# Performance work log

Measured on AMD Instinct MI355X. Metric: run time of the kernel, lower is better.

## Reference

```python
import jax, jax.numpy as jnp
import numpy as np

B, S, HID = 2, 2048, 2048
H, KVH, HD = 16, 8, 128
EPS = 1e-6
ROPE_THETA = 1e6
NEG = -1e9


def setup_inputs() -> dict:
    key = jax.random.key(0)
    ks = jax.random.split(key, 8)
    hidden_states = jax.random.normal(ks[0], (B, S, HID), dtype=jnp.float32)
    # real rotary embeddings, HF layout: concat(freqs, freqs) along last dim
    inv_freq = 1.0 / (ROPE_THETA ** (jnp.arange(0, HD, 2, dtype=jnp.float32) / HD))
    freqs = jnp.arange(S, dtype=jnp.float32)[:, None] * inv_freq[None, :]  # [S, HD/2]
    emb = jnp.concatenate([freqs, freqs], axis=-1)  # [S, HD]
    cos = jnp.broadcast_to(jnp.cos(emb)[None], (B, S, HD)).astype(jnp.float32)
    sin = jnp.broadcast_to(jnp.sin(emb)[None], (B, S, HD)).astype(jnp.float32)
    # additive causal mask [B, 1, S, S]
    causal = jnp.tril(jnp.ones((S, S), dtype=bool))
    attention_mask = jnp.broadcast_to(
        jnp.where(causal, 0.0, NEG).astype(jnp.float32)[None, None], (B, 1, S, S)
    )
    sc_in = 1.0 / np.sqrt(HID)
    sc_o = 1.0 / np.sqrt(H * HD)
    q_kernel = jax.random.normal(ks[1], (HID, H * HD), dtype=jnp.float32) * sc_in
    k_kernel = jax.random.normal(ks[2], (HID, KVH * HD), dtype=jnp.float32) * sc_in
    v_kernel = jax.random.normal(ks[3], (HID, KVH * HD), dtype=jnp.float32) * sc_in
    o_kernel = jax.random.normal(ks[4], (H * HD, HID), dtype=jnp.float32) * sc_o
    q_norm_w = jnp.ones((HD,), dtype=jnp.float32)
    k_norm_w = jnp.ones((HD,), dtype=jnp.float32)
    return dict(hidden_states=hidden_states, cos=cos, sin=sin,
                attention_mask=attention_mask, q_kernel=q_kernel, k_kernel=k_kernel,
                v_kernel=v_kernel, o_kernel=o_kernel, q_norm_w=q_norm_w, k_norm_w=k_norm_w)


def _rms_norm(x, w):
    dt = x.dtype
    xf = x.astype(jnp.float32)
    var = jnp.mean(jnp.square(xf), axis=-1, keepdims=True)
    return (w * (xf * jax.lax.rsqrt(var + EPS))).astype(dt)


def _rotate_half(x):
    x1, x2 = jnp.split(x, 2, axis=-1)
    return jnp.concatenate([-x2, x1], axis=-1)


def _apply_rope(q, k, cos, sin):
    # q,k: [B,H,S,HD]; cos,sin: [B,S,HD] -> unsqueeze head dim
    cos = cos[:, None, :, :]
    sin = sin[:, None, :, :]
    q = q * cos + _rotate_half(q) * sin
    k = k * cos + _rotate_half(k) * sin
    return q, k


def reference(hidden_states, cos, sin, attention_mask, q_kernel, k_kernel,
              v_kernel, o_kernel, q_norm_w, k_norm_w):
    b, s, _ = hidden_states.shape
    groups = H // KVH
    scaling = HD ** -0.5

    q = (hidden_states @ q_kernel).reshape(b, s, H, HD).transpose(0, 2, 1, 3)
    k = (hidden_states @ k_kernel).reshape(b, s, KVH, HD).transpose(0, 2, 1, 3)
    v = (hidden_states @ v_kernel).reshape(b, s, KVH, HD).transpose(0, 2, 1, 3)

    q = _rms_norm(q, q_norm_w)
    k = _rms_norm(k, k_norm_w)
    q, k = _apply_rope(q, k, cos, sin)

    # GQA repeat_kv: [B,KVH,S,HD] -> [B,H,S,HD]
    k = jnp.repeat(k, groups, axis=1)
    v = jnp.repeat(v, groups, axis=1)

    attn = jnp.einsum('bhqd,bhkd->bhqk', q, k) * scaling  # [B,H,S,S]
    attn = attn + jnp.broadcast_to(attention_mask[:, :, :, :s], (b, H, s, s))
    attn = jax.nn.softmax(attn, axis=-1)
    out = jnp.einsum('bhqk,bhkd->bhqd', attn, v)
    out = out.transpose(0, 2, 1, 3).reshape(b, s, H * HD)
    return out @ o_kernel
```

## Files before the change

kernel.cpp:

```cpp
#include <hip/hip_runtime.h>
#include <hip/hip_bf16.h>
#include <stdint.h>

#define S_ 2048
#define H_ 16
#define KVH_ 8
#define HD_ 128

typedef short bf16x8 __attribute__((ext_vector_type(8)));
typedef float f32x4 __attribute__((ext_vector_type(4)));

__device__ __forceinline__ unsigned short f2bf(float f) {
    union { float f; uint32_t u; } v; v.f = f;
    uint32_t u = v.u;
    return (unsigned short)((u + 0x7FFFu + ((u >> 16) & 1u)) >> 16);
}
__device__ __forceinline__ float bf2f(unsigned short s) {
    union { uint32_t u; float f; } v; v.u = ((uint32_t)s) << 16;
    return v.f;
}
__device__ __forceinline__ void gload16(const void* g, void* l) {
    __builtin_amdgcn_global_load_lds(
        (const __attribute__((address_space(1))) unsigned int*)(uintptr_t)g,
        (__attribute__((address_space(3))) unsigned int*)(unsigned int)(uintptr_t)l,
        16, 0, 0);
}
__device__ __forceinline__ float rowred_sum(float x) {
    float t;
    t = __int_as_float(__builtin_amdgcn_update_dpp(0, __float_as_int(x), 0x121, 0xF, 0xF, true)); x += t;
    t = __int_as_float(__builtin_amdgcn_update_dpp(0, __float_as_int(x), 0x122, 0xF, 0xF, true)); x += t;
    t = __int_as_float(__builtin_amdgcn_update_dpp(0, __float_as_int(x), 0x124, 0xF, 0xF, true)); x += t;
    t = __int_as_float(__builtin_amdgcn_update_dpp(0, __float_as_int(x), 0x128, 0xF, 0xF, true)); x += t;
    return x;
}

__global__ __launch_bounds__(256) void k_prep(
    const float* __restrict__ hidden, unsigned short* __restrict__ Xb,
    const float* __restrict__ qk, const float* __restrict__ kk,
    const float* __restrict__ vk, const float* __restrict__ ok,
    unsigned short* __restrict__ Wqkvt, unsigned short* __restrict__ Wot) {
    const int tid = threadIdx.x;
    if (blockIdx.x < 2048) {
        int i = blockIdx.x * 256 + tid;
        const int stride = 2048 * 256;
        #pragma unroll
        for (int u = 0; u < 4; u++, i += stride) {
            float4 f = ((const float4*)hidden)[i];
            ushort4 o;
            o.x = f2bf(f.x); o.y = f2bf(f.y); o.z = f2bf(f.z); o.w = f2bf(f.w);
            ((ushort4*)Xb)[i] = o;
        }
    } else {
        __shared__ float tile[32][33];
        const int t = blockIdx.x - 2048;
        const float* src; unsigned short* dst; int N, bx, by;
        if (t < 4096)      { src = qk; dst = Wqkvt;                          N = 2048; bx = t & 63; by = t >> 6; }
        else if (t < 6144) { int u = t - 4096; src = kk; dst = Wqkvt + (size_t)2048 * 2048; N = 1024; bx = u & 31; by = u >> 5; }
        else if (t < 8192) { int u = t - 6144; src = vk; dst = Wqkvt + (size_t)3072 * 2048; N = 1024; bx = u & 31; by = u >> 5; }
        else               { int u = t - 8192; src = ok; dst = Wot;          N = 2048; bx = u & 63; by = u >> 6; }
        const int n0 = bx * 32, k0 = by * 32;
        const int tx = tid & 31, ty = tid >> 5;
        #pragma unroll
        for (int j = 0; j < 32; j += 8)
            tile[ty + j][tx] = src[(size_t)(k0 + ty + j) * N + n0 + tx];
        __syncthreads();
        #pragma unroll
        for (int j = 0; j < 32; j += 8)
            dst[(size_t)(n0 + ty + j) * 2048 + k0 + tx] = f2bf(tile[tx][ty + j]);
    }
}

template <int BM, int OUT_F32>
__global__ __launch_bounds__(512) void k_gemm256(const unsigned short* __restrict__ A,
                                                 const unsigned short* __restrict__ Bt,
                                                 void* __restrict__ Cv,
                                                 int M, int N, int K) {
    __shared__ __align__(16) unsigned short As[2][BM * 32];
    __shared__ __align__(16) unsigned short Bs[2][256 * 32];
    const int tid = threadIdx.x;
    const int wave = tid >> 6, lane = tid & 63;
    const int lm = lane & 15, lg = lane >> 4;
    const int wr = wave >> 2, wc = wave & 3;
    const int m0 = blockIdx.y * BM, n0 = blockIdx.x * 256;
    constexpr int MF = BM / 32;
    f32x4 acc[MF][4] = {};
    const int srow = wave * 16 + (lane >> 2);
    const int sslot = (lane & 3) ^ ((lane >> 3) & 3);
    const unsigned short* gA = A + (size_t)(m0 + srow) * K + sslot * 8;
    const unsigned short* gB = Bt + (size_t)(n0 + srow) * K + sslot * 8;
    const int swz = lg ^ ((lm >> 1) & 3);
    const int NKT = K >> 5;

    auto STAGE = [&](int kt, int buf) {
        const int c = kt * 32;
        char* lA = (char*)&As[buf][0] + wave * 1024;
        char* lB = (char*)&Bs[buf][0] + wave * 1024;
        gload16(gA + c, lA);
        if constexpr (BM == 256) gload16(gA + c + (size_t)128 * K, lA + 8192);
        gload16(gB + c, lB);
        gload16(gB + c + (size_t)128 * K, lB + 8192);
    };
    STAGE(0, 0);
    for (int kt = 0; kt < NKT; ++kt) {
        const int cur = kt & 1;
        if (kt + 1 < NKT) {
            STAGE(kt + 1, cur ^ 1);
            __builtin_amdgcn_sched_barrier(0);
            if constexpr (BM == 256) asm volatile("s_waitcnt vmcnt(4)" ::: "memory");
            else                     asm volatile("s_waitcnt vmcnt(3)" ::: "memory");
        } else {
            __builtin_amdgcn_sched_barrier(0);
            asm volatile("s_waitcnt vmcnt(0)" ::: "memory");
        }
        __builtin_amdgcn_s_barrier();
        __builtin_amdgcn_sched_barrier(0);
        bf16x8 bfr[4];
        #pragma unroll
        for (int n = 0; n < 4; n++)
            bfr[n] = *(const bf16x8*)&Bs[cur][(wc * 64 + n * 16 + lm) * 32 + swz * 8];
        __builtin_amdgcn_s_setprio(1);
        #pragma unroll
        for (int m = 0; m < MF; m++) {
            bf16x8 a = *(const bf16x8*)&As[cur][(wr * (BM / 2) + m * 16 + lm) * 32 + swz * 8];
            #pragma unroll
            for (int n = 0; n < 4; n++)
                acc[m][n] = __builtin_amdgcn_mfma_f32_16x16x32_bf16(a, bfr[n], acc[m][n], 0, 0, 0);
        }
        __builtin_amdgcn_s_setprio(0);
        __builtin_amdgcn_sched_barrier(0);
        __builtin_amdgcn_s_barrier();
        __builtin_amdgcn_sched_barrier(0);
    }
    #pragma unroll
    for (int m = 0; m < MF; m++) {
        const int row = m0 + wr * (BM / 2) + m * 16 + lg * 4;
        #pragma unroll
        for (int n = 0; n < 4; n++) {
            const int col = n0 + wc * 64 + n * 16 + lm;
            #pragma unroll
            for (int i = 0; i < 4; i++) {
                if (OUT_F32) ((float*)Cv)[(size_t)(row + i) * N + col] = acc[m][n][i];
                else ((unsigned short*)Cv)[(size_t)(row + i) * N + col] = f2bf(acc[m][n][i]);
            }
        }
    }
}

__global__ __launch_bounds__(256) void k_normvt(
    const unsigned short* __restrict__ Cqkv,
    const float* __restrict__ cosb, const float* __restrict__ sinb,
    const float* __restrict__ qw, const float* __restrict__ kw,
    unsigned short* __restrict__ Qb, unsigned short* __restrict__ Kb,
    unsigned short* __restrict__ Vtg) {
    const int tid = threadIdx.x;
    if (blockIdx.x < 4096) {
        const int row = blockIdx.x;
        const int b = row >> 11, s = row & (S_ - 1);
        const int wave = tid >> 6, lane = tid & 63;
        const float c0 = cosb[(size_t)row * HD_ + lane];
        const float c1 = cosb[(size_t)row * HD_ + lane + 64];
        const float s0 = sinb[(size_t)row * HD_ + lane];
        const float s1 = sinb[(size_t)row * HD_ + lane + 64];
        for (int u = wave; u < 24; u += 4) {
            const int isq = (u < 16);
            const int head = isq ? u : u - 16;
            const unsigned short* x = Cqkv + (size_t)row * 4096 + (isq ? 0 : 2048) + head * HD_;
            float x0 = bf2f(x[lane]), x1 = bf2f(x[lane + 64]);
            float ss = x0 * x0 + x1 * x1;
            #pragma unroll
            for (int o = 32; o >= 1; o >>= 1) ss += __shfl_xor(ss, o, 64);
            float r = rsqrtf(ss * (1.0f / HD_) + 1e-6f);
            const float* wv = isq ? qw : kw;
            float y0 = x0 * r * wv[lane], y1 = x1 * r * wv[lane + 64];
            float o0 = y0 * c0 - y1 * s0;
            float o1 = y1 * c1 + y0 * s1;
            unsigned short* dst = isq ? Qb + ((size_t)(b * H_ + head) * S_ + s) * HD_
                                      : Kb + ((size_t)(b * KVH_ + head) * S_ + s) * HD_;
            dst[lane] = f2bf(o0);
            dst[lane + 64] = f2bf(o1);
        }
    } else {
        __shared__ unsigned short tile[32][34];
        const int t = blockIdx.x - 4096;
        const int x = t & 63, y = (t >> 6) & 3, bkh = t >> 8;
        const int b = bkh >> 3, kh = bkh & 7;
        const int s0 = x * 32, d0 = y * 32;
        const int tx = tid & 31, ty = tid >> 5;
        #pragma unroll
        for (int j = 0; j < 32; j += 8)
            tile[ty + j][tx] = Cqkv[(size_t)(b * S_ + s0 + ty + j) * 4096 + 3072 + kh * HD_ + d0 + tx];
        __syncthreads();
        #pragma unroll
        for (int j = 0; j < 32; j += 8)
            Vtg[((size_t)bkh * HD_ + d0 + ty + j) * S_ + s0 + tx] = tile[tx][ty + j];
    }
}

__global__ __launch_bounds__(256) void k_attn(
    const unsigned short* __restrict__ Qb,
    const unsigned short* __restrict__ Kb,
    const unsigned short* __restrict__ Vtg,
    unsigned short* __restrict__ AO) {
    __shared__ __align__(16) unsigned short Kt[2][64 * 128];
    __shared__ __align__(16) unsigned short Vt[2][128 * 64];
    __shared__ __align__(16) unsigned short Pl[4][16][72];
    const int h = blockIdx.y, b = blockIdx.z;
    const int qi = (b == 0) ? (gridDim.x - 1 - blockIdx.x) : blockIdx.x;
    const int kh = h >> 1;
    const int tid = threadIdx.x, wave = tid >> 6, lane = tid & 63;
    const int lm = lane & 15, lg = lane >> 4;
    const int q0 = qi * 128;
    bf16x8 qf[2][4];
    #pragma unroll
    for (int rg = 0; rg < 2; rg++) {
        const unsigned short* Qp = Qb + ((size_t)(b * H_ + h) * S_ + q0 + wave * 32 + rg * 16 + lm) * HD_;
        #pragma unroll
        for (int d0 = 0; d0 < 4; d0++) qf[rg][d0] = *(const bf16x8*)(Qp + d0 * 32 + lg * 8);
    }
    f32x4 accO[2][8] = {};
    float lrow[2][4];
    #pragma unroll
    for (int rg = 0; rg < 2; rg++)
        #pragma unroll
        for (int i = 0; i < 4; i++) lrow[rg][i] = 0.f;
    const unsigned short* Kg = Kb + (size_t)(b * KVH_ + kh) * S_ * HD_;
    const unsigned short* Vg = Vtg + (size_t)(b * KVH_ + kh) * HD_ * S_;
    const int kr = wave * 4 + (lane >> 4);
    const int kc = ((lane & 15) ^ (kr & 7)) * 8;
    const int vr = wave * 8 + (lane >> 3);
    const int vc = ((lane & 7) ^ (vr & 7)) * 8;
    const float scaling = 0.08838834764831845f;
    const int NT = 2 * qi + 2;

    auto STAGE = [&](int t, int buf) {
        const int k0 = t * 64;
        char* lK = (char*)&Kt[buf][0] + wave * 1024;
        char* lV = (char*)&Vt[buf][0] + wave * 1024;
        #pragma unroll
        for (int j = 0; j < 4; ++j) {
            gload16(Kg + (size_t)(k0 + kr + j * 16) * HD_ + kc, lK + j * 4096);
            gload16(Vg + (size_t)(vr + j * 32) * S_ + k0 + vc, lV + j * 4096);
        }
    };
    STAGE(0, 0);
    for (int t = 0; t < NT; ++t) {
        const int cur = t & 1;
        const int k0 = t * 64;
        if (t + 1 < NT) {
            STAGE(t + 1, cur ^ 1);
            __builtin_amdgcn_sched_barrier(0);
            asm volatile("s_waitcnt vmcnt(8)" ::: "memory");
        } else {
            __builtin_amdgcn_sched_barrier(0);
            asm volatile("s_waitcnt vmcnt(0)" ::: "memory");
        }
        __builtin_amdgcn_s_barrier();
        __builtin_amdgcn_sched_barrier(0);
        f32x4 sc[2][4] = {};
        __builtin_amdgcn_s_setprio(1);
        #pragma unroll
        for (int nk = 0; nk < 4; nk++)
            #pragma unroll
            for (int d0 = 0; d0 < 4; d0++) {
                bf16x8 kf = *(const bf16x8*)&Kt[cur][(nk * 16 + lm) * 128 +
                                                    ((d0 * 32 + lg * 8) ^ ((lm & 7) << 3))];
                sc[0][nk] = __builtin_amdgcn_mfma_f32_16x16x32_bf16(qf[0][d0], kf, sc[0][nk], 0, 0, 0);
                sc[1][nk] = __builtin_amdgcn_mfma_f32_16x16x32_bf16(qf[1][d0], kf, sc[1][nk], 0, 0, 0);
            }
        __builtin_amdgcn_s_setprio(0);
        const bool diag = (t >= 2 * qi);
        #pragma unroll
        for (int rg = 0; rg < 2; rg++) {
            const int qrow0 = q0 + wave * 32 + rg * 16;
            float rs[4] = { 0.f, 0.f, 0.f, 0.f };
            #pragma unroll
            for (int nk = 0; nk < 4; nk++)
                #pragma unroll
                for (int i = 0; i < 4; i++) {
                    float v = sc[rg][nk][i] * scaling;
                    if (diag && (k0 + nk * 16 + lm) > (qrow0 + lg * 4 + i)) v = -1e30f;
                    float p = __expf(v);
                    rs[i] += p;
                    Pl[wave][lg * 4 + i][nk * 16 + lm] = f2bf(p);
                }
            #pragma unroll
            for (int i = 0; i < 4; i++) rs[i] = rowred_sum(rs[i]);
            #pragma unroll
            for (int i = 0; i < 4; i++) lrow[rg][i] += rs[i];
            __builtin_amdgcn_s_setprio(1);
            #pragma unroll
            for (int kk = 0; kk < 2; kk++) {
                bf16x8 pa = *(const bf16x8*)&Pl[wave][lm][kk * 32 + lg * 8];
                #pragma unroll
                for (int df = 0; df < 8; df++) {
                    bf16x8 vf = *(const bf16x8*)&Vt[cur][(df * 16 + lm) * 64 +
                                                         ((kk * 32 + lg * 8) ^ ((lm & 7) << 3))];
                    accO[rg][df] = __builtin_amdgcn_mfma_f32_16x16x32_bf16(pa, vf, accO[rg][df], 0, 0, 0);
                }
            }
            __builtin_amdgcn_s_setprio(0);
        }
        __builtin_amdgcn_sched_barrier(0);
        __builtin_amdgcn_s_barrier();
        __builtin_amdgcn_sched_barrier(0);
    }
    #pragma unroll
    for (int rg = 0; rg < 2; rg++) {
        unsigned short* Op = AO + ((size_t)b * S_ + q0 + wave * 32 + rg * 16) * (H_ * HD_) + h * HD_;
        #pragma unroll
        for (int df = 0; df < 8; df++)
            #pragma unroll
            for (int i = 0; i < 4; i++) {
                float v = accO[rg][df][i] / lrow[rg][i];
                Op[(size_t)(lg * 4 + i) * (H_ * HD_) + df * 16 + lm] = f2bf(v);
            }
    }
}

extern "C" void kernel_launch(void* const* d_in, const int* in_sizes, int n_in,
                              void* d_out, int out_size, void* d_ws, size_t ws_size,
                              hipStream_t stream) {
    const float* hidden = (const float*)d_in[0];
    const float* cosb = (const float*)d_in[1];
    const float* sinb = (const float*)d_in[2];
    const float* qk = (const float*)d_in[4];
    const float* kk = (const float*)d_in[5];
    const float* vk = (const float*)d_in[6];
    const float* ok = (const float*)d_in[7];
    const float* qw = (const float*)d_in[8];
    const float* kw = (const float*)d_in[9];
    char* ws = (char*)d_ws;
    unsigned short* Xb    = (unsigned short*)ws;
    unsigned short* Wqkvt = (unsigned short*)(ws + (16u << 20));
    unsigned short* Wot   = (unsigned short*)(ws + (32u << 20));
    unsigned short* Cqkv  = (unsigned short*)(ws + (40u << 20));
    unsigned short* Qb  = Xb;
    unsigned short* Kb  = Wqkvt;
    unsigned short* Vtg = (unsigned short*)(ws + (24u << 20));
    unsigned short* AO  = Cqkv;

    k_prep<<<14336, 256, 0, stream>>>(hidden, Xb, qk, kk, vk, ok, Wqkvt, Wot);
    k_gemm256<256, 0><<<dim3(16, 16), 512, 0, stream>>>(Xb, Wqkvt, Cqkv, 4096, 4096, 2048);
    k_normvt<<<8192, 256, 0, stream>>>(Cqkv, cosb, sinb, qw, kw, Qb, Kb, Vtg);
    k_attn<<<dim3(16, H_, 2), 256, 0, stream>>>(Qb, Kb, Vtg, AO);
    k_gemm256<128, 1><<<dim3(8, 32), 512, 0, stream>>>(AO, Wot, d_out, 4096, 2048, 2048);
}
```

Before: 239.5 us.

## Halve attention query tile and split K/V staging into single-buffered interleaved loads

```diff
diff --git a/kernel.cpp b/kernel.cpp
--- a/kernel.cpp
+++ b/kernel.cpp
@@ -201,28 +201,21 @@
     const unsigned short* __restrict__ Kb,
     const unsigned short* __restrict__ Vtg,
     unsigned short* __restrict__ AO) {
-    __shared__ __align__(16) unsigned short Kt[2][64 * 128];
-    __shared__ __align__(16) unsigned short Vt[2][128 * 64];
+    __shared__ __align__(16) unsigned short Kt[64 * 128];
+    __shared__ __align__(16) unsigned short Vt[128 * 64];
     __shared__ __align__(16) unsigned short Pl[4][16][72];
     const int h = blockIdx.y, b = blockIdx.z;
-    const int qi = (b == 0) ? (gridDim.x - 1 - blockIdx.x) : blockIdx.x;
+    const int qi = gridDim.x - 1 - blockIdx.x;
     const int kh = h >> 1;
     const int tid = threadIdx.x, wave = tid >> 6, lane = tid & 63;
     const int lm = lane & 15, lg = lane >> 4;
-    const int q0 = qi * 128;
-    bf16x8 qf[2][4];
+    const int q0 = qi * 64;
+    const unsigned short* Qp = Qb + ((size_t)(b * H_ + h) * S_ + q0 + wave * 16 + lm) * HD_;
+    bf16x8 qf[4];
     #pragma unroll
-    for (int rg = 0; rg < 2; rg++) {
-        const unsigned short* Qp = Qb + ((size_t)(b * H_ + h) * S_ + q0 + wave * 32 + rg * 16 + lm) * HD_;
-        #pragma unroll
-        for (int d0 = 0; d0 < 4; d0++) qf[rg][d0] = *(const bf16x8*)(Qp + d0 * 32 + lg * 8);
-    }
-    f32x4 accO[2][8] = {};
-    float lrow[2][4];
-    #pragma unroll
-    for (int rg = 0; rg < 2; rg++)
-        #pragma unroll
-        for (int i = 0; i < 4; i++) lrow[rg][i] = 0.f;
+    for (int d0 = 0; d0 < 4; d0++) qf[d0] = *(const bf16x8*)(Qp + d0 * 32 + lg * 8);
+    f32x4 accO[8] = {};
+    float lrow[4] = { 0.f, 0.f, 0.f, 0.f };
     const unsigned short* Kg = Kb + (size_t)(b * KVH_ + kh) * S_ * HD_;
     const unsigned short* Vg = Vtg + (size_t)(b * KVH_ + kh) * HD_ * S_;
     const int kr = wave * 4 + (lane >> 4);
@@ -230,91 +223,92 @@
     const int vr = wave * 8 + (lane >> 3);
     const int vc = ((lane & 7) ^ (vr & 7)) * 8;
     const float scaling = 0.08838834764831845f;
-    const int NT = 2 * qi + 2;
-
-    auto STAGE = [&](int t, int buf) {
+    const int NT = qi + 1;
+
+    auto STAGE_K = [&](int t) {
         const int k0 = t * 64;
-        char* lK = (char*)&Kt[buf][0] + wave * 1024;
-        char* lV = (char*)&Vt[buf][0] + wave * 1024;
-        #pragma unroll
-        for (int j = 0; j < 4; ++j) {
+        char* lK = (char*)&Kt[0] + wave * 1024;
+        #pragma unroll
+        for (int j = 0; j < 4; ++j)
             gload16(Kg + (size_t)(k0 + kr + j * 16) * HD_ + kc, lK + j * 4096);
+    };
+    auto STAGE_V = [&](int t) {
+        const int k0 = t * 64;
+        char* lV = (char*)&Vt[0] + wave * 1024;
+        #pragma unroll
+        for (int j = 0; j < 4; ++j)
             gload16(Vg + (size_t)(vr + j * 32) * S_ + k0 + vc, lV + j * 4096);
-        }
     };
-    STAGE(0, 0);
+    STAGE_K(0);
+    STAGE_V(0);
     for (int t = 0; t < NT; ++t) {
-        const int cur = t & 1;
         const int k0 = t * 64;
-        if (t + 1 < NT) {
-            STAGE(t + 1, cur ^ 1);
-            __builtin_amdgcn_sched_barrier(0);
-            asm volatile("s_waitcnt vmcnt(8)" ::: "memory");
-        } else {
-            __builtin_amdgcn_sched_barrier(0);
-            asm volatile("s_waitcnt vmcnt(0)" ::: "memory");
-        }
-        __builtin_amdgcn_s_barrier();
-        __builtin_amdgcn_sched_barrier(0);
-        f32x4 sc[2][4] = {};
+        __builtin_amdgcn_sched_barrier(0);
+        asm volatile("s_waitcnt vmcnt(4)" ::: "memory");
+        __builtin_amdgcn_s_barrier();
+        __builtin_amdgcn_sched_barrier(0);
+        f32x4 sc[4] = {};
         __builtin_amdgcn_s_setprio(1);
         #pragma unroll
         for (int nk = 0; nk < 4; nk++)
             #pragma unroll
             for (int d0 = 0; d0 < 4; d0++) {
-                bf16x8 kf = *(const bf16x8*)&Kt[cur][(nk * 16 + lm) * 128 +
-                                                    ((d0 * 32 + lg * 8) ^ ((lm & 7) << 3))];
-                sc[0][nk] = __builtin_amdgcn_mfma_f32_16x16x32_bf16(qf[0][d0], kf, sc[0][nk], 0, 0, 0);
-                sc[1][nk] = __builtin_amdgcn_mfma_f32_16x16x32_bf16(qf[1][d0], kf, sc[1][nk], 0, 0, 0);
+                bf16x8 kf = *(const bf16x8*)&Kt[(nk * 16 + lm) * 128 +
+                                               ((d0 * 32 + lg * 8) ^ ((lm & 7) << 3))];
+                sc[nk] = __builtin_amdgcn_mfma_f32_16x16x32_bf16(qf[d0], kf, sc[nk], 0, 0, 0);
             }
         __builtin_amdgcn_s_setprio(0);
-        const bool diag = (t >= 2 * qi);
-        #pragma unroll
-        for (int rg = 0; rg < 2; rg++) {
-            const int qrow0 = q0 + wave * 32 + rg * 16;
-            float rs[4] = { 0.f, 0.f, 0.f, 0.f };
-            #pragma unroll
-            for (int nk = 0; nk < 4; nk++)
-                #pragma unroll
-                for (int i = 0; i < 4; i++) {
-                    float v = sc[rg][nk][i] * scaling;
-                    if (diag && (k0 + nk * 16 + lm) > (qrow0 + lg * 4 + i)) v = -1e30f;
-                    float p = __expf(v);
-                    rs[i] += p;
-                    Pl[wave][lg * 4 + i][nk * 16 + lm] = f2bf(p);
-                }
-            #pragma unroll
-            for (int i = 0; i < 4; i++) rs[i] = rowred_sum(rs[i]);
-            #pragma unroll
-            for (int i = 0; i < 4; i++) lrow[rg][i] += rs[i];
-            __builtin_amdgcn_s_setprio(1);
-            #pragma unroll
-            for (int kk = 0; kk < 2; kk++) {
-                bf16x8 pa = *(const bf16x8*)&Pl[wave][lm][kk * 32 + lg * 8];
-                #pragma unroll
-                for (int df = 0; df < 8; df++) {
-                    bf16x8 vf = *(const bf16x8*)&Vt[cur][(df * 16 + lm) * 64 +
-                                                         ((kk * 32 + lg * 8) ^ ((lm & 7) << 3))];
-                    accO[rg][df] = __builtin_amdgcn_mfma_f32_16x16x32_bf16(pa, vf, accO[rg][df], 0, 0, 0);
-                }
+        __builtin_amdgcn_sched_barrier(0);
+        __builtin_amdgcn_s_barrier();
+        __builtin_amdgcn_sched_barrier(0);
+        if (t + 1 < NT) STAGE_K(t + 1);
+        const bool diag = (t == qi);
+        const int qrow0 = q0 + wave * 16;
+        float rs[4] = { 0.f, 0.f, 0.f, 0.f };
+        #pragma unroll
+        for (int nk = 0; nk < 4; nk++)
+            #pragma unroll
+            for (int i = 0; i < 4; i++) {
+                float v = sc[nk][i] * scaling;
+                if (diag && (k0 + nk * 16 + lm) > (qrow0 + lg * 4 + i)) v = -1e30f;
+                float p = __expf(v);
+                rs[i] += p;
+                Pl[wave][lg * 4 + i][nk * 16 + lm] = f2bf(p);
             }
-            __builtin_amdgcn_s_setprio(0);
-        }
-        __builtin_amdgcn_sched_barrier(0);
-        __builtin_amdgcn_s_barrier();
-        __builtin_amdgcn_sched_barrier(0);
-    }
+        #pragma unroll
+        for (int i = 0; i < 4; i++) rs[i] = rowred_sum(rs[i]);
+        #pragma unroll
+        for (int i = 0; i < 4; i++) lrow[i] += rs[i];
+        __builtin_amdgcn_sched_barrier(0);
+        if (t + 1 < NT) { asm volatile("s_waitcnt vmcnt(4)" ::: "memory"); }
+        else            { asm volatile("s_waitcnt vmcnt(0)" ::: "memory"); }
+        __builtin_amdgcn_s_barrier();
+        __builtin_amdgcn_sched_barrier(0);
+        __builtin_amdgcn_s_setprio(1);
+        #pragma unroll
+        for (int kk = 0; kk < 2; kk++) {
+            bf16x8 pa = *(const bf16x8*)&Pl[wave][lm][kk * 32 + lg * 8];
+            #pragma unroll
+            for (int df = 0; df < 8; df++) {
+                bf16x8 vf = *(const bf16x8*)&Vt[(df * 16 + lm) * 64 +
+                                               ((kk * 32 + lg * 8) ^ ((lm & 7) << 3))];
+                accO[df] = __builtin_amdgcn_mfma_f32_16x16x32_bf16(pa, vf, accO[df], 0, 0, 0);
+            }
+        }
+        __builtin_amdgcn_s_setprio(0);
+        __builtin_amdgcn_sched_barrier(0);
+        __builtin_amdgcn_s_barrier();
+        __builtin_amdgcn_sched_barrier(0);
+        if (t + 1 < NT) STAGE_V(t + 1);
+    }
+    unsigned short* Op = AO + ((size_t)b * S_ + q0 + wave * 16) * (H_ * HD_) + h * HD_;
     #pragma unroll
-    for (int rg = 0; rg < 2; rg++) {
-        unsigned short* Op = AO + ((size_t)b * S_ + q0 + wave * 32 + rg * 16) * (H_ * HD_) + h * HD_;
-        #pragma unroll
-        for (int df = 0; df < 8; df++)
-            #pragma unroll
-            for (int i = 0; i < 4; i++) {
-                float v = accO[rg][df][i] / lrow[rg][i];
-                Op[(size_t)(lg * 4 + i) * (H_ * HD_) + df * 16 + lm] = f2bf(v);
-            }
-    }
+    for (int df = 0; df < 8; df++)
+        #pragma unroll
+        for (int i = 0; i < 4; i++) {
+            float v = accO[df][i] / lrow[i];
+            Op[(size_t)(lg * 4 + i) * (H_ * HD_) + df * 16 + lm] = f2bf(v);
+        }
 }
 
 extern "C" void kernel_launch(void* const* d_in, const int* in_sizes, int n_in,
@@ -342,6 +336,6 @@
     k_prep<<<14336, 256, 0, stream>>>(hidden, Xb, qk, kk, vk, ok, Wqkvt, Wot);
     k_gemm256<256, 0><<<dim3(16, 16), 512, 0, stream>>>(Xb, Wqkvt, Cqkv, 4096, 4096, 2048);
     k_normvt<<<8192, 256, 0, stream>>>(Cqkv, cosb, sinb, qw, kw, Qb, Kb, Vtg);
-    k_attn<<<dim3(16, H_, 2), 256, 0, stream>>>(Qb, Kb, Vtg, AO);
+    k_attn<<<dim3(32, H_, 2), 256, 0, stream>>>(Qb, Kb, Vtg, AO);
     k_gemm256<128, 1><<<dim3(8, 32), 512, 0, stream>>>(AO, Wot, d_out, 4096, 2048, 2048);
 }
```

New measurement: 270.8 us. +13.0%, slower.
